# Optimization experiments

Measured on AMD Instinct MI355X. Metric: run time of the kernel, lower is better.

The kernel has to match this reference:

```python
import jax, jax.numpy as jnp
import numpy as np

B, N, D, H = 4, 512, 4, 256


def _linear_params(key, fan_in, fan_out):
    # torch.nn.Linear default init: U(-1/sqrt(fan_in), 1/sqrt(fan_in))
    lim = 1.0 / np.sqrt(fan_in)
    kw, kb = jax.random.split(key)
    W = jax.random.uniform(kw, (fan_in, fan_out), minval=-lim, maxval=lim, dtype=jnp.float32)
    b = jax.random.uniform(kb, (fan_out,), minval=-lim, maxval=lim, dtype=jnp.float32)
    return W, b


def setup_inputs() -> dict:
    key = jax.random.key(0)
    ks = jax.random.split(key, 8)
    x = jax.random.normal(ks[0], (B, N, D), dtype=jnp.float32)
    adj = jax.random.uniform(ks[1], (B, N, N), dtype=jnp.float32)  # soft adjacency in [0,1)
    W_e1, b_e1 = _linear_params(ks[2], 2 * D, H)
    W_e2, b_e2 = _linear_params(ks[3], H, H)
    W_n1, b_n1 = _linear_params(ks[4], H, H)
    W_n2, b_n2 = _linear_params(ks[5], H, H)
    W_o1, b_o1 = _linear_params(ks[6], D + H, H)
    W_o, b_o = _linear_params(ks[7], H, D)
    return {
        "x": x, "adj": adj,
        "W_e1": W_e1, "b_e1": b_e1, "W_e2": W_e2, "b_e2": b_e2,
        "W_n1": W_n1, "b_n1": b_n1, "W_n2": W_n2, "b_n2": b_n2,
        "W_o1": W_o1, "b_o1": b_o1, "W_o": W_o, "b_o": b_o,
    }


def reference(x, adj, W_e1, b_e1, W_e2, b_e2, W_n1, b_n1, W_n2, b_n2, W_o1, b_o1, W_o, b_o):
    b_, n_, d_ = x.shape
    # innode[b,i,j,:] = x[b,j]; outnode[b,i,j,:] = x[b,i]
    innode = jnp.broadcast_to(x[:, None, :, :], (b_, n_, n_, d_))
    outnode = jnp.broadcast_to(x[:, :, None, :], (b_, n_, n_, d_))
    edge_in = jnp.concatenate([innode, outnode], axis=-1)          # [B,N,N,2D]
    node2edge = jax.nn.relu(edge_in @ W_e1 + b_e1)                 # [B,N,N,H]
    edge2edge = jax.nn.relu(node2edge @ W_e2 + b_e2)               # [B,N,N,H]
    # adjacency-masked sum over axis 1 (the i axis)
    agg = jnp.einsum('bij,bijh->bjh', adj, edge2edge)              # [B,N,H]
    out1 = jax.nn.relu(agg @ W_n1 + b_n1)
    out2 = jax.nn.relu(out1 @ W_n2 + b_n2)
    out3 = jnp.concatenate([x, out2], axis=-1)                     # [B,N,D+H]
    out4 = out3 @ W_o1 + b_o1
    out5 = out4 @ W_o + b_o                                        # [B,N,D]
    # CONTINUOUS is False for the classifier variant
    return jax.nn.log_softmax(out5, axis=2)
```

## Files before the change

### kernel.cpp

```cpp
#include <hip/hip_runtime.h>
#include <hip/hip_fp16.h>
#include <math.h>

#define Bq 4
#define Nq 512
#define Dq 4
#define Hq 256

typedef _Float16 f16x8 __attribute__((ext_vector_type(8)));
typedef float f32x4 __attribute__((ext_vector_type(4)));

__device__ __forceinline__ f16x8 hadd_relu(f16x8 u, f16x8 v) {
    f16x8 s = u + v;
    const f16x8 z = (f16x8)(_Float16)0.0f;
    return __builtin_elementwise_max(s, z);
}

__global__ __launch_bounds__(256) void prep_uv(
    const float* __restrict__ x, const float* __restrict__ We1,
    const float* __restrict__ be1, __half* __restrict__ U, __half* __restrict__ V) {
    const int bn = blockIdx.x;
    const int k = threadIdx.x;
    const float* xp = x + bn * Dq;
    const float x0 = xp[0], x1 = xp[1], x2 = xp[2], x3 = xp[3];
    float u = be1[k];
    u = fmaf(x0, We1[0 * 256 + k], u);
    u = fmaf(x1, We1[1 * 256 + k], u);
    u = fmaf(x2, We1[2 * 256 + k], u);
    u = fmaf(x3, We1[3 * 256 + k], u);
    float v = x0 * We1[4 * 256 + k];
    v = fmaf(x1, We1[5 * 256 + k], v);
    v = fmaf(x2, We1[6 * 256 + k], v);
    v = fmaf(x3, We1[7 * 256 + k], v);
    U[(size_t)bn * Hq + k] = __float2half(u);
    V[(size_t)bn * Hq + k] = __float2half(v);
}

__global__ __launch_bounds__(256, 2) void edge_gemm(
    const __half* __restrict__ U, const __half* __restrict__ V,
    const float* __restrict__ We2, const float* __restrict__ be2,
    const float* __restrict__ adj, float* __restrict__ aggws) {
    __shared__ __align__(16) __half Wt[64 * 256];
    __shared__ __align__(16) __half Us[16 * 256];
    __shared__ __align__(16) __half Vs[16 * 256];
    __shared__ float adjs[16 * 16];

    const int bid = blockIdx.x;
    const int hq_ = bid & 3;
    const int jt = (bid >> 2) & 31;
    const int b = bid >> 7;
    const int h_base = hq_ * 64;
    const int j_base = jt * 16;
    const int t = threadIdx.x;
    const int lane = t & 63;
    const int w = t >> 6;
    const int q = lane >> 4;
    const int l15 = lane & 15;

    {
        const int n = t & 63;
        const int swz = n & 31;
        for (int kk = (t >> 6); kk < 256; kk += 4) {
            float val = We2[kk * 256 + h_base + n];
            Wt[n * 256 + ((((kk >> 3) ^ swz)) << 3) + (kk & 7)] = __float2half(val);
        }
    }
    {
        const int row = t >> 4;
        const int c0 = (t & 15) * 2;
        const uint4* gp = (const uint4*)(U + (size_t)(b * Nq + j_base + row) * Hq);
        uint4 v0 = gp[c0];
        uint4 v1 = gp[c0 + 1];
        *(uint4*)&Us[row * 256 + ((c0 ^ row) << 3)] = v0;
        *(uint4*)&Us[row * 256 + (((c0 + 1) ^ row) << 3)] = v1;
    }

    float bias[4];
#pragma unroll
    for (int nt = 0; nt < 4; ++nt) bias[nt] = be2[h_base + nt * 16 + l15];

    f32x4 agg[4];
#pragma unroll
    for (int nt = 0; nt < 4; ++nt) agg[nt] = (f32x4){0.f, 0.f, 0.f, 0.f};

    for (int ch = 0; ch < 32; ++ch) {
        const int i_base = ch * 16;
        __syncthreads();
        {
            const int row = t >> 4;
            const int c0 = (t & 15) * 2;
            const uint4* gp = (const uint4*)(V + (size_t)(b * Nq + i_base + row) * Hq);
            uint4 v0 = gp[c0];
            uint4 v1 = gp[c0 + 1];
            *(uint4*)&Vs[row * 256 + ((c0 ^ row) << 3)] = v0;
            *(uint4*)&Vs[row * 256 + (((c0 + 1) ^ row) << 3)] = v1;
        }
        adjs[t] = adj[(size_t)(b * Nq + i_base + (t >> 4)) * Nq + j_base + (t & 15)];
        __syncthreads();

        f32x4 acc[4][4];
#pragma unroll
        for (int mi = 0; mi < 4; ++mi)
#pragma unroll
            for (int nt = 0; nt < 4; ++nt)
                acc[mi][nt] = (f32x4){bias[nt], bias[nt], bias[nt], bias[nt]};

#pragma unroll
        for (int ks = 0; ks < 8; ++ks) {
            const int c = ks * 4 + q;
            const f16x8 uvec = *(const f16x8*)&Us[l15 * 256 + ((c ^ l15) << 3)];
            f16x8 afrag[4];
#pragma unroll
            for (int mi = 0; mi < 4; ++mi) {
                const int iv = w * 4 + mi;
                const f16x8 vvec = *(const f16x8*)&Vs[iv * 256 + ((c ^ iv) << 3)];
                afrag[mi] = hadd_relu(uvec, vvec);
            }
            f16x8 bfrag[4];
#pragma unroll
            for (int nt = 0; nt < 4; ++nt) {
                const int rn = nt * 16 + l15;
                bfrag[nt] = *(const f16x8*)&Wt[rn * 256 + ((c ^ (rn & 31)) << 3)];
            }
#pragma unroll
            for (int mi = 0; mi < 4; ++mi)
#pragma unroll
                for (int nt = 0; nt < 4; ++nt)
                    acc[mi][nt] = __builtin_amdgcn_mfma_f32_16x16x32_f16(
                        afrag[mi], bfrag[nt], acc[mi][nt], 0, 0, 0);
        }

#pragma unroll
        for (int mi = 0; mi < 4; ++mi) {
            const int iv = w * 4 + mi;
            const float a0 = adjs[iv * 16 + q * 4 + 0];
            const float a1 = adjs[iv * 16 + q * 4 + 1];
            const float a2 = adjs[iv * 16 + q * 4 + 2];
            const float a3 = adjs[iv * 16 + q * 4 + 3];
#pragma unroll
            for (int nt = 0; nt < 4; ++nt) {
                agg[nt][0] = fmaf(a0, fmaxf(acc[mi][nt][0], 0.f), agg[nt][0]);
                agg[nt][1] = fmaf(a1, fmaxf(acc[mi][nt][1], 0.f), agg[nt][1]);
                agg[nt][2] = fmaf(a2, fmaxf(acc[mi][nt][2], 0.f), agg[nt][2]);
                agg[nt][3] = fmaf(a3, fmaxf(acc[mi][nt][3], 0.f), agg[nt][3]);
            }
        }
    }

#pragma unroll
    for (int nt = 0; nt < 4; ++nt)
#pragma unroll
        for (int r = 0; r < 4; ++r) {
            const int j = j_base + q * 4 + r;
            const int h = h_base + nt * 16 + l15;
            atomicAdd(&aggws[(size_t)(b * Nq + j) * Hq + h], agg[nt][r]);
        }
}

__global__ __launch_bounds__(256) void tail_kernel(
    const float* __restrict__ aggws, const float* __restrict__ x,
    const float* __restrict__ Wn1, const float* __restrict__ bn1,
    const float* __restrict__ Wn2, const float* __restrict__ bn2,
    const float* __restrict__ Wo1, const float* __restrict__ bo1,
    const float* __restrict__ Wo, const float* __restrict__ bo,
    float* __restrict__ out) {
    __shared__ __align__(16) float bufA[256 * 4];
    __shared__ __align__(16) float bufB[256 * 4];
    __shared__ float xs[4][4];
    __shared__ float s5[4][4];
    const int bid = blockIdx.x;
    const int b = bid >> 7;
    const int n0 = (bid & 127) * 4;
    const int t = threadIdx.x;

#pragma unroll
    for (int ni = 0; ni < 4; ++ni)
        bufA[t * 4 + ni] = aggws[(size_t)(b * Nq + n0 + ni) * Hq + t];
    if (t < 16) xs[t >> 2][t & 3] = x[(size_t)(b * Nq + n0 + (t >> 2)) * Dq + (t & 3)];
    __syncthreads();

    float c0, c1, c2, c3;
    c0 = c1 = c2 = c3 = bn1[t];
    for (int k = 0; k < 256; ++k) {
        const float wv = Wn1[k * 256 + t];
        const float4 av = *(const float4*)&bufA[k * 4];
        c0 = fmaf(av.x, wv, c0); c1 = fmaf(av.y, wv, c1);
        c2 = fmaf(av.z, wv, c2); c3 = fmaf(av.w, wv, c3);
    }
    bufB[t * 4 + 0] = fmaxf(c0, 0.f); bufB[t * 4 + 1] = fmaxf(c1, 0.f);
    bufB[t * 4 + 2] = fmaxf(c2, 0.f); bufB[t * 4 + 3] = fmaxf(c3, 0.f);
    __syncthreads();

    c0 = c1 = c2 = c3 = bn2[t];
    for (int k = 0; k < 256; ++k) {
        const float wv = Wn2[k * 256 + t];
        const float4 av = *(const float4*)&bufB[k * 4];
        c0 = fmaf(av.x, wv, c0); c1 = fmaf(av.y, wv, c1);
        c2 = fmaf(av.z, wv, c2); c3 = fmaf(av.w, wv, c3);
    }
    bufA[t * 4 + 0] = fmaxf(c0, 0.f); bufA[t * 4 + 1] = fmaxf(c1, 0.f);
    bufA[t * 4 + 2] = fmaxf(c2, 0.f); bufA[t * 4 + 3] = fmaxf(c3, 0.f);
    __syncthreads();

    c0 = c1 = c2 = c3 = bo1[t];
#pragma unroll
    for (int d = 0; d < 4; ++d) {
        const float wv = Wo1[d * 256 + t];
        c0 = fmaf(xs[0][d], wv, c0); c1 = fmaf(xs[1][d], wv, c1);
        c2 = fmaf(xs[2][d], wv, c2); c3 = fmaf(xs[3][d], wv, c3);
    }
    for (int k = 0; k < 256; ++k) {
        const float wv = Wo1[(4 + k) * 256 + t];
        const float4 av = *(const float4*)&bufA[k * 4];
        c0 = fmaf(av.x, wv, c0); c1 = fmaf(av.y, wv, c1);
        c2 = fmaf(av.z, wv, c2); c3 = fmaf(av.w, wv, c3);
    }
    bufB[t * 4 + 0] = c0; bufB[t * 4 + 1] = c1;
    bufB[t * 4 + 2] = c2; bufB[t * 4 + 3] = c3;
    __syncthreads();

    const int d = t >> 6;
    const int lane = t & 63;
    float p0 = 0.f, p1 = 0.f, p2 = 0.f, p3 = 0.f;
    for (int k = lane; k < 256; k += 64) {
        const float wv = Wo[k * 4 + d];
        const float4 av = *(const float4*)&bufB[k * 4];
        p0 = fmaf(av.x, wv, p0); p1 = fmaf(av.y, wv, p1);
        p2 = fmaf(av.z, wv, p2); p3 = fmaf(av.w, wv, p3);
    }
#pragma unroll
    for (int off = 32; off > 0; off >>= 1) {
        p0 += __shfl_down(p0, off); p1 += __shfl_down(p1, off);
        p2 += __shfl_down(p2, off); p3 += __shfl_down(p3, off);
    }
    if (lane == 0) {
        s5[0][d] = p0 + bo[d]; s5[1][d] = p1 + bo[d];
        s5[2][d] = p2 + bo[d]; s5[3][d] = p3 + bo[d];
    }
    __syncthreads();
    if (t < 4) {
        const float v0 = s5[t][0], v1 = s5[t][1], v2 = s5[t][2], v3 = s5[t][3];
        const float m = fmaxf(fmaxf(v0, v1), fmaxf(v2, v3));
        const float s = expf(v0 - m) + expf(v1 - m) + expf(v2 - m) + expf(v3 - m);
        const float lse = m + logf(s);
        float* op = out + (size_t)(b * Nq + n0 + t) * Dq;
        op[0] = v0 - lse; op[1] = v1 - lse; op[2] = v2 - lse; op[3] = v3 - lse;
    }
}

extern "C" void kernel_launch(void* const* d_in, const int* in_sizes, int n_in,
                              void* d_out, int out_size, void* d_ws, size_t ws_size,
                              hipStream_t stream) {
    const float* x   = (const float*)d_in[0];
    const float* adj = (const float*)d_in[1];
    const float* We1 = (const float*)d_in[2];
    const float* be1 = (const float*)d_in[3];
    const float* We2 = (const float*)d_in[4];
    const float* be2 = (const float*)d_in[5];
    const float* Wn1 = (const float*)d_in[6];
    const float* bn1 = (const float*)d_in[7];
    const float* Wn2 = (const float*)d_in[8];
    const float* bn2 = (const float*)d_in[9];
    const float* Wo1 = (const float*)d_in[10];
    const float* bo1 = (const float*)d_in[11];
    const float* Wo  = (const float*)d_in[12];
    const float* bo  = (const float*)d_in[13];
    float* out = (float*)d_out;

    __half* U = (__half*)d_ws;
    __half* V = U + (size_t)Bq * Nq * Hq;
    float* aggws = (float*)((char*)d_ws + (size_t)2 * Bq * Nq * Hq * sizeof(__half));

    (void)hipMemsetAsync(aggws, 0, (size_t)Bq * Nq * Hq * sizeof(float), stream);
    prep_uv<<<Bq * Nq, 256, 0, stream>>>(x, We1, be1, U, V);
    edge_gemm<<<512, 256, 0, stream>>>(U, V, We2, be2, adj, aggws);
    tail_kernel<<<512, 256, 0, stream>>>(aggws, x, Wn1, bn1, Wn2, bn2, Wo1, bo1, Wo, bo, out);
}
```

Measured before the change: 250.8 us.

## Hoist W fragments into registers and replace atomics with in-block reduction

The edge GEMM now loads all B-operand fragments of the W_e2 tile into registers once before the i-chunk loop, so they are no longer re-read from LDS every chunk. The per-warp partial aggregates are reduced through shared memory (aliased over the weight tile) and written with plain vector stores, which removes the global atomics and the memset of the aggregation buffer. The adjacency read becomes a vector load, and the tail kernel's loops get unroll hints. This costs 128 extra VGPRs for the fragments, which risks spilling or lower occupancy under the launch bound of 2 blocks.

```diff
diff --git a/kernel.cpp b/kernel.cpp
--- a/kernel.cpp
+++ b/kernel.cpp
@@ -40,10 +40,12 @@
     const __half* __restrict__ U, const __half* __restrict__ V,
     const float* __restrict__ We2, const float* __restrict__ be2,
     const float* __restrict__ adj, float* __restrict__ aggws) {
-    __shared__ __align__(16) __half Wt[64 * 256];
-    __shared__ __align__(16) __half Us[16 * 256];
-    __shared__ __align__(16) __half Vs[16 * 256];
-    __shared__ float adjs[16 * 16];
+    __shared__ __align__(16) char smem[50176];
+    __half* Wt = (__half*)smem;
+    __half* Us = (__half*)(smem + 32768);
+    __half* Vs = (__half*)(smem + 40960);
+    float* adjs = (float*)(smem + 49152);
+    float* red = (float*)smem;
 
     const int bid = blockIdx.x;
     const int hq_ = bid & 3;
@@ -74,6 +76,18 @@
         *(uint4*)&Us[row * 256 + ((c0 ^ row) << 3)] = v0;
         *(uint4*)&Us[row * 256 + (((c0 + 1) ^ row) << 3)] = v1;
     }
+    __syncthreads();
+
+    f16x8 bfrag[4][8];
+#pragma unroll
+    for (int nt = 0; nt < 4; ++nt) {
+        const int rn = nt * 16 + l15;
+#pragma unroll
+        for (int ks = 0; ks < 8; ++ks) {
+            const int c = ks * 4 + q;
+            bfrag[nt][ks] = *(const f16x8*)&Wt[rn * 256 + ((c ^ (rn & 31)) << 3)];
+        }
+    }
 
     float bias[4];
 #pragma unroll
@@ -116,33 +130,24 @@
                 const f16x8 vvec = *(const f16x8*)&Vs[iv * 256 + ((c ^ iv) << 3)];
                 afrag[mi] = hadd_relu(uvec, vvec);
             }
-            f16x8 bfrag[4];
-#pragma unroll
-            for (int nt = 0; nt < 4; ++nt) {
-                const int rn = nt * 16 + l15;
-                bfrag[nt] = *(const f16x8*)&Wt[rn * 256 + ((c ^ (rn & 31)) << 3)];
-            }
 #pragma unroll
             for (int mi = 0; mi < 4; ++mi)
 #pragma unroll
                 for (int nt = 0; nt < 4; ++nt)
                     acc[mi][nt] = __builtin_amdgcn_mfma_f32_16x16x32_f16(
-                        afrag[mi], bfrag[nt], acc[mi][nt], 0, 0, 0);
+                        afrag[mi], bfrag[nt][ks], acc[mi][nt], 0, 0, 0);
         }
 
 #pragma unroll
         for (int mi = 0; mi < 4; ++mi) {
             const int iv = w * 4 + mi;
-            const float a0 = adjs[iv * 16 + q * 4 + 0];
-            const float a1 = adjs[iv * 16 + q * 4 + 1];
-            const float a2 = adjs[iv * 16 + q * 4 + 2];
-            const float a3 = adjs[iv * 16 + q * 4 + 3];
+            const f32x4 av = *(const f32x4*)&adjs[iv * 16 + q * 4];
 #pragma unroll
             for (int nt = 0; nt < 4; ++nt) {
-                agg[nt][0] = fmaf(a0, fmaxf(acc[mi][nt][0], 0.f), agg[nt][0]);
-                agg[nt][1] = fmaf(a1, fmaxf(acc[mi][nt][1], 0.f), agg[nt][1]);
-                agg[nt][2] = fmaf(a2, fmaxf(acc[mi][nt][2], 0.f), agg[nt][2]);
-                agg[nt][3] = fmaf(a3, fmaxf(acc[mi][nt][3], 0.f), agg[nt][3]);
+                agg[nt][0] = fmaf(av[0], fmaxf(acc[mi][nt][0], 0.f), agg[nt][0]);
+                agg[nt][1] = fmaf(av[1], fmaxf(acc[mi][nt][1], 0.f), agg[nt][1]);
+                agg[nt][2] = fmaf(av[2], fmaxf(acc[mi][nt][2], 0.f), agg[nt][2]);
+                agg[nt][3] = fmaf(av[3], fmaxf(acc[mi][nt][3], 0.f), agg[nt][3]);
             }
         }
     }
@@ -150,11 +155,18 @@
 #pragma unroll
     for (int nt = 0; nt < 4; ++nt)
 #pragma unroll
-        for (int r = 0; r < 4; ++r) {
-            const int j = j_base + q * 4 + r;
-            const int h = h_base + nt * 16 + l15;
-            atomicAdd(&aggws[(size_t)(b * Nq + j) * Hq + h], agg[nt][r]);
-        }
+        for (int r = 0; r < 4; ++r)
+            red[w * 1024 + (q * 4 + r) * 64 + nt * 16 + l15] = agg[nt][r];
+    __syncthreads();
+    {
+        const int j = t >> 4;
+        const int h0 = (t & 15) * 4;
+        f32x4 s = *(const f32x4*)&red[0 * 1024 + j * 64 + h0];
+        s += *(const f32x4*)&red[1 * 1024 + j * 64 + h0];
+        s += *(const f32x4*)&red[2 * 1024 + j * 64 + h0];
+        s += *(const f32x4*)&red[3 * 1024 + j * 64 + h0];
+        *(f32x4*)&aggws[(size_t)(b * Nq + j_base + j) * Hq + h_base + h0] = s;
+    }
 }
 
 __global__ __launch_bounds__(256) void tail_kernel(
@@ -181,6 +193,7 @@
 
     float c0, c1, c2, c3;
     c0 = c1 = c2 = c3 = bn1[t];
+#pragma unroll 8
     for (int k = 0; k < 256; ++k) {
         const float wv = Wn1[k * 256 + t];
         const float4 av = *(const float4*)&bufA[k * 4];
@@ -192,6 +205,7 @@
     __syncthreads();
 
     c0 = c1 = c2 = c3 = bn2[t];
+#pragma unroll 8
     for (int k = 0; k < 256; ++k) {
         const float wv = Wn2[k * 256 + t];
         const float4 av = *(const float4*)&bufB[k * 4];
@@ -209,6 +223,7 @@
         c0 = fmaf(xs[0][d], wv, c0); c1 = fmaf(xs[1][d], wv, c1);
         c2 = fmaf(xs[2][d], wv, c2); c3 = fmaf(xs[3][d], wv, c3);
     }
+#pragma unroll 8
     for (int k = 0; k < 256; ++k) {
         const float wv = Wo1[(4 + k) * 256 + t];
         const float4 av = *(const float4*)&bufA[k * 4];
@@ -271,7 +286,6 @@
     __half* V = U + (size_t)Bq * Nq * Hq;
     float* aggws = (float*)((char*)d_ws + (size_t)2 * Bq * Nq * Hq * sizeof(__half));
 
-    (void)hipMemsetAsync(aggws, 0, (size_t)Bq * Nq * Hq * sizeof(float), stream);
     prep_uv<<<Bq * Nq, 256, 0, stream>>>(x, We1, be1, U, V);
     edge_gemm<<<512, 256, 0, stream>>>(U, V, We2, be2, adj, aggws);
     tail_kernel<<<512, 256, 0, stream>>>(aggws, x, Wn1, bn1, Wn2, bn2, Wo1, bo1, Wo, bo, out);
```

Measured after the change: 410.1 us. 1.64x slower.
